# Performance work log

Measured on AMD Instinct MI355X. Metric: run time of the kernel, lower is better.

The kernel has to match this reference:

```python
import jax, jax.numpy as jnp
import numpy as np

B, S, NN = 16, 512, 8          # batch, spatial nodes, neighbors per node
IN, H, NHEAD = 128, 512, 4     # input_size, hidden_size, n_head


def _forward(inputs, h, c, h_spatial, a_src, w_fg, b_fg, w_ig, b_ig,
             w_ih, w_hh, b_ih, b_hh):
    N = B * S
    x = inputs.reshape(N, IN)
    h = h.reshape(N, H)
    c = c.reshape(N, H)
    hs = h_spatial.reshape(N, NN, H)

    # attention logits: concat(h, neighbor) @ a_src, split to avoid materializing concat
    a_self, a_nb = a_src[:H], a_src[H:]              # [H, NHEAD] each
    attn = h @ a_self                                  # [N, NHEAD]
    attn = attn[:, None, :] + jnp.einsum('nkh,hm->nkm', hs, a_nb)  # [N, NN, NHEAD]
    attn = jnp.where(attn >= 0, attn, 0.2 * attn)      # leaky_relu(0.2)
    attn = jax.nn.softmax(attn, axis=1)                # softmax over neighbors

    # aggregate neighbors per head -> [N, NHEAD*H]
    agg = jnp.einsum('nkm,nkh->nmh', attn, hs).reshape(N, NHEAD * H)

    spatial_f = jax.nn.sigmoid(agg @ w_fg.T + b_fg)    # [N, H]
    spatial_i = jax.nn.sigmoid(agg @ w_ig.T + b_ig)
    h = h * spatial_i
    c = c * spatial_f

    # torch LSTMCell: gate order i, f, g, o
    gates = x @ w_ih.T + b_ih + h @ w_hh.T + b_hh      # [N, 4H]
    i_g, f_g, g_g, o_g = jnp.split(gates, 4, axis=1)
    i_g = jax.nn.sigmoid(i_g)
    f_g = jax.nn.sigmoid(f_g)
    g_g = jnp.tanh(g_g)
    o_g = jax.nn.sigmoid(o_g)
    c_new = f_g * c + i_g * g_g
    h_new = o_g * jnp.tanh(c_new)
    return h_new.reshape(B, S, H), c_new.reshape(B, S, H)


def setup_inputs() -> dict:
    key = jax.random.key(0)
    ks = jax.random.split(key, 16)
    xav = lambda k, shp: jax.random.uniform(
        k, shp, jnp.float32, -1.0, 1.0) * np.sqrt(6.0 / (shp[0] + shp[1]))
    return {
        'inputs': jax.random.normal(ks[0], (B, S, IN), jnp.float32),
        'h': jax.random.normal(ks[1], (B, S, H), jnp.float32),
        'c': jax.random.normal(ks[2], (B, S, H), jnp.float32),
        'h_spatial': jax.random.normal(ks[3], (B, S, NN, H), jnp.float32),
        'a_src': xav(ks[4], (2 * H, NHEAD)),
        'w_fg': jax.random.normal(ks[5], (H, NHEAD * H), jnp.float32) * 0.02,
        'b_fg': jnp.zeros((H,), jnp.float32),
        'w_ig': jax.random.normal(ks[6], (H, NHEAD * H), jnp.float32) * 0.02,
        'b_ig': jnp.zeros((H,), jnp.float32),
        'w_ih': jax.random.normal(ks[7], (4 * H, IN), jnp.float32) * 0.02,
        'w_hh': jax.random.normal(ks[8], (4 * H, H), jnp.float32) * 0.02,
        'b_ih': jnp.zeros((4 * H,), jnp.float32),
        'b_hh': jnp.zeros((4 * H,), jnp.float32),
    }


def reference(inputs, h, c, h_spatial, a_src, w_fg, b_fg, w_ig, b_ig,
              w_ih, w_hh, b_ih, b_hh):
    return _forward(inputs, h, c, h_spatial, a_src, w_fg, b_fg, w_ig, b_ig,
                    w_ih, w_hh, b_ih, b_hh)
```

## Files before the change

### kernel.cpp

```cpp
#include <hip/hip_runtime.h>
#include <hip/hip_bf16.h>
#include <cstdint>
#include <cstddef>

#define N_ROWS 8192
#define HDIM 512
#define INDIM 128
#define NHEADS 4
#define NNB 8

typedef __bf16 bf16_t;
typedef __bf16 bf16x8 __attribute__((ext_vector_type(8)));
typedef __bf16 bf16x4 __attribute__((ext_vector_type(4)));
typedef __bf16 bf16x2 __attribute__((ext_vector_type(2)));
typedef float f32x4 __attribute__((ext_vector_type(4)));

__device__ __forceinline__ float sigmoidf_(float x) { return 1.0f / (1.0f + expf(-x)); }

__device__ __forceinline__ void load_lds16(const void* g, void* l) {
  __builtin_amdgcn_global_load_lds(
      (const __attribute__((address_space(1))) void*)g,
      (__attribute__((address_space(3))) void*)l, 16, 0, 0);
}

__global__ __launch_bounds__(256) void pack_kernel(
    const float* __restrict__ w_fg, const float* __restrict__ w_ig,
    const float* __restrict__ w_ih, const float* __restrict__ w_hh,
    const float* __restrict__ b_ih, const float* __restrict__ b_hh,
    const float* __restrict__ x,
    bf16_t* __restrict__ W1, bf16_t* __restrict__ W2i,
    float* __restrict__ b2, bf16_t* __restrict__ A2)
{
  int idx = blockIdx.x * 256 + threadIdx.x;
  if (idx < 524288) {
    const int e = idx * 4, r = e >> 11, k = e & 2047;
    const float* src = (r < 512) ? &w_fg[(size_t)r * 2048 + k]
                                 : &w_ig[(size_t)(r - 512) * 2048 + k];
    const float4 v = *(const float4*)src;
    bf16x4 o; o[0] = (bf16_t)v.x; o[1] = (bf16_t)v.y; o[2] = (bf16_t)v.z; o[3] = (bf16_t)v.w;
    *(bf16x4*)&W1[e] = o;
    return;
  }
  idx -= 524288;
  if (idx < 327680) {
    const int e = idx * 4, r = e / 640, k = e - r * 640;
    const int rp = (r & 511) * 4 + (r >> 9);
    const float* src = (k < 128) ? &w_ih[(size_t)r * 128 + k]
                                 : &w_hh[(size_t)r * 512 + (k - 128)];
    const float4 v = *(const float4*)src;
    bf16x4 o; o[0] = (bf16_t)v.x; o[1] = (bf16_t)v.y; o[2] = (bf16_t)v.z; o[3] = (bf16_t)v.w;
    *(bf16x4*)&W2i[(size_t)rp * 640 + k] = o;
    return;
  }
  idx -= 327680;
  if (idx < 2048) {
    const int q = idx >> 2, g = idx & 3;
    b2[idx] = b_ih[g * 512 + q] + b_hh[g * 512 + q];
    return;
  }
  idx -= 2048;
  if (idx < 262144) {
    const int e = idx * 4, n = e >> 7, cc = e & 127;
    const float4 v = *(const float4*)&x[e];
    bf16x4 o; o[0] = (bf16_t)v.x; o[1] = (bf16_t)v.y; o[2] = (bf16_t)v.z; o[3] = (bf16_t)v.w;
    *(bf16x4*)&A2[(size_t)n * 640 + cc] = o;
  }
}

__global__ __launch_bounds__(256) void attn_agg_kernel(
    const float* __restrict__ h, const float* __restrict__ hs,
    const float* __restrict__ a_src, bf16_t* __restrict__ agg)
{
  __shared__ float s_hs[NNB][HDIM];
  __shared__ float s_h[HDIM];
  __shared__ float s_logit[NNB][NHEADS];
  __shared__ float s_self[NHEADS];

  const int n = blockIdx.x;
  const int t = threadIdx.x;
  const float* hs_n = hs + (size_t)n * (NNB * HDIM);
  const float* h_n  = h  + (size_t)n * HDIM;

  {
    const float4* s4 = (const float4*)hs_n;
    float4* d4 = (float4*)&s_hs[0][0];
#pragma unroll
    for (int i = 0; i < 4; ++i) d4[t + i * 256] = s4[t + i * 256];
    if (t < HDIM / 4) ((float4*)s_h)[t] = ((const float4*)h_n)[t];
  }
  __syncthreads();

  const int wave = t >> 6, lane = t & 63;
#pragma unroll
  for (int kk = 0; kk < 2; ++kk) {
    const int k = wave * 2 + kk;
    float acc0 = 0.f, acc1 = 0.f, acc2 = 0.f, acc3 = 0.f;
#pragma unroll
    for (int i = 0; i < HDIM / 64; ++i) {
      const int hh = i * 64 + lane;
      const float v = s_hs[k][hh];
      const float4 av = *(const float4*)(a_src + (size_t)(HDIM + hh) * NHEADS);
      acc0 += v * av.x; acc1 += v * av.y; acc2 += v * av.z; acc3 += v * av.w;
    }
    float accs[NHEADS] = {acc0, acc1, acc2, acc3};
#pragma unroll
    for (int m = 0; m < NHEADS; ++m) {
      float a = accs[m];
#pragma unroll
      for (int off = 32; off > 0; off >>= 1) a += __shfl_xor(a, off);
      if (lane == 0) s_logit[k][m] = a;
    }
  }
  if (wave == 0) {
    float acc0 = 0.f, acc1 = 0.f, acc2 = 0.f, acc3 = 0.f;
#pragma unroll
    for (int i = 0; i < HDIM / 64; ++i) {
      const int hh = i * 64 + lane;
      const float v = s_h[hh];
      const float4 av = *(const float4*)(a_src + (size_t)hh * NHEADS);
      acc0 += v * av.x; acc1 += v * av.y; acc2 += v * av.z; acc3 += v * av.w;
    }
    float accs[NHEADS] = {acc0, acc1, acc2, acc3};
#pragma unroll
    for (int m = 0; m < NHEADS; ++m) {
      float a = accs[m];
#pragma unroll
      for (int off = 32; off > 0; off >>= 1) a += __shfl_xor(a, off);
      if (lane == 0) s_self[m] = a;
    }
  }
  __syncthreads();

  float w[NNB][NHEADS];
#pragma unroll
  for (int m = 0; m < NHEADS; ++m) {
    const float sm = s_self[m];
    float mx = -1e30f;
#pragma unroll
    for (int k = 0; k < NNB; ++k) {
      float l = sm + s_logit[k][m];
      l = (l >= 0.f) ? l : 0.2f * l;
      w[k][m] = l;
      mx = fmaxf(mx, l);
    }
    float sum = 0.f;
#pragma unroll
    for (int k = 0; k < NNB; ++k) { const float e = expf(w[k][m] - mx); w[k][m] = e; sum += e; }
    const float inv = 1.f / sum;
#pragma unroll
    for (int k = 0; k < NNB; ++k) w[k][m] *= inv;
  }

  bf16_t* agg_n = agg + (size_t)n * (NHEADS * HDIM);
  const int hh = t * 2;
  float e0[NNB], e1[NNB];
#pragma unroll
  for (int k = 0; k < NNB; ++k) { e0[k] = s_hs[k][hh]; e1[k] = s_hs[k][hh + 1]; }
#pragma unroll
  for (int m = 0; m < NHEADS; ++m) {
    float a0 = 0.f, a1 = 0.f;
#pragma unroll
    for (int k = 0; k < NNB; ++k) { a0 += w[k][m] * e0[k]; a1 += w[k][m] * e1[k]; }
    bf16x2 pk; pk[0] = (bf16_t)a0; pk[1] = (bf16_t)a1;
    *(bf16x2*)(agg_n + m * HDIM + hh) = pk;
  }
}

__global__ __launch_bounds__(256) void gemm1_kernel(
    const bf16_t* __restrict__ A, const bf16_t* __restrict__ Bt,
    const float* __restrict__ b_fg, const float* __restrict__ b_ig,
    const float* __restrict__ c_in, const float* __restrict__ h_in,
    float* __restrict__ cprime, bf16_t* __restrict__ A2)
{
  __shared__ bf16_t At[2][128][32];
  __shared__ bf16_t Bs[2][64][32];

  const int tid  = threadIdx.x;
  const int wave = tid >> 6, lane = tid & 63;
  const int wr = wave >> 1, wc = wave & 1;
  const int bm0 = blockIdx.x * 128;
  const int bn0 = blockIdx.y * 64;
  const int K = 2048;

  f32x4 acc[4][2] = {};

  const int srow = tid >> 2;
  const int sch  = tid & 3;
  const int gsw8 = (sch ^ ((srow >> 1) & 3)) * 8;
  const int sch8 = sch * 8;
  const int frow = lane & 15;
  const int fro8 = ((lane >> 4) ^ ((frow >> 1) & 3)) * 8;

  auto STAGE = [&](int buf, int k0) {
    load_lds16(A  + (size_t)(bm0 + srow)      * K + k0 + gsw8, &At[buf][srow][sch8]);
    load_lds16(A  + (size_t)(bm0 + 64 + srow) * K + k0 + gsw8, &At[buf][64 + srow][sch8]);
    load_lds16(Bt + (size_t)(bn0 + srow)      * K + k0 + gsw8, &Bs[buf][srow][sch8]);
  };
  auto COMPUTE = [&](int buf) {
    bf16x8 af[4], bv[2];
#pragma unroll
    for (int i = 0; i < 4; ++i) af[i] = *(const bf16x8*)&At[buf][wr * 64 + i * 16 + frow][fro8];
#pragma unroll
    for (int j = 0; j < 2; ++j) bv[j] = *(const bf16x8*)&Bs[buf][wc * 32 + j * 16 + frow][fro8];
#pragma unroll
    for (int i = 0; i < 4; ++i)
#pragma unroll
      for (int j = 0; j < 2; ++j)
        acc[i][j] = __builtin_amdgcn_mfma_f32_16x16x32_bf16(af[i], bv[j], acc[i][j], 0, 0, 0);
  };

  const int nt = K >> 5;
  STAGE(0, 0);
  __syncthreads();
  for (int t = 0; t < nt; ++t) {
    if (t + 1 < nt) STAGE((t + 1) & 1, (t + 1) * 32);
    COMPUTE(t & 1);
    __syncthreads();
  }

  const int col_in = lane & 15;
  const int row_in = (lane >> 4) * 4;
#pragma unroll
  for (int i = 0; i < 4; ++i) {
#pragma unroll
    for (int j = 0; j < 2; ++j) {
      const int col = bn0 + wc * 32 + j * 16 + col_in;
#pragma unroll
      for (int r = 0; r < 4; ++r) {
        const int row = bm0 + wr * 64 + i * 16 + row_in + r;
        const float v = acc[i][j][r];
        if (col < 512) {
          const float s = sigmoidf_(v + b_fg[col]);
          cprime[(size_t)row * 512 + col] = c_in[(size_t)row * 512 + col] * s;
        } else {
          const int jj = col - 512;
          const float s = sigmoidf_(v + b_ig[jj]);
          A2[(size_t)row * 640 + 128 + jj] = (bf16_t)(h_in[(size_t)row * 512 + jj] * s);
        }
      }
    }
  }
}

__global__ __launch_bounds__(256) void gemm2_kernel(
    const bf16_t* __restrict__ A, const bf16_t* __restrict__ Bt,
    const float* __restrict__ b2, const float* __restrict__ cprime,
    float* __restrict__ out)
{
  __shared__ union {
    struct { bf16_t A[2][128][32]; bf16_t B[2][128][32]; } st;
    float epi[64][128];
  } sm;

  const int tid  = threadIdx.x;
  const int wave = tid >> 6, lane = tid & 63;
  const int wr = wave >> 1, wc = wave & 1;
  const int bm0 = blockIdx.x * 128;
  const int bn0 = blockIdx.y * 128;
  const int K = 640;

  f32x4 acc[4][4] = {};

  const int srow = tid >> 2;
  const int sch  = tid & 3;
  const int gsw8 = (sch ^ ((srow >> 1) & 3)) * 8;
  const int sch8 = sch * 8;
  const int frow = lane & 15;
  const int fro8 = ((lane >> 4) ^ ((frow >> 1) & 3)) * 8;

  auto STAGE = [&](int buf, int k0) {
    load_lds16(A  + (size_t)(bm0 + srow)      * K + k0 + gsw8, &sm.st.A[buf][srow][sch8]);
    load_lds16(A  + (size_t)(bm0 + 64 + srow) * K + k0 + gsw8, &sm.st.A[buf][64 + srow][sch8]);
    load_lds16(Bt + (size_t)(bn0 + srow)      * K + k0 + gsw8, &sm.st.B[buf][srow][sch8]);
    load_lds16(Bt + (size_t)(bn0 + 64 + srow) * K + k0 + gsw8, &sm.st.B[buf][64 + srow][sch8]);
  };
  auto COMPUTE = [&](int buf) {
    bf16x8 af[4], bv[4];
#pragma unroll
    for (int i = 0; i < 4; ++i) af[i] = *(const bf16x8*)&sm.st.A[buf][wr * 64 + i * 16 + frow][fro8];
#pragma unroll
    for (int j = 0; j < 4; ++j) bv[j] = *(const bf16x8*)&sm.st.B[buf][wc * 64 + j * 16 + frow][fro8];
#pragma unroll
    for (int i = 0; i < 4; ++i)
#pragma unroll
      for (int j = 0; j < 4; ++j)
        acc[i][j] = __builtin_amdgcn_mfma_f32_16x16x32_bf16(af[i], bv[j], acc[i][j], 0, 0, 0);
  };

  const int nt = K >> 5;
  STAGE(0, 0);
  __syncthreads();
  for (int t = 0; t < nt; ++t) {
    if (t + 1 < nt) STAGE((t + 1) & 1, (t + 1) * 32);
    COMPUTE(t & 1);
    __syncthreads();
  }

  const int col_in = lane & 15;
  const int row_in = (lane >> 4) * 4;
  const int q0i = bn0 >> 2;
  const int qi  = tid & 31;
  const int r0  = tid >> 5;

#pragma unroll
  for (int p = 0; p < 2; ++p) {
    if (wr == p) {
#pragma unroll
      for (int i = 0; i < 4; ++i)
#pragma unroll
        for (int j = 0; j < 4; ++j)
#pragma unroll
          for (int r = 0; r < 4; ++r)
            sm.epi[i * 16 + row_in + r][wc * 64 + j * 16 + col_in] = acc[i][j][r];
    }
    __syncthreads();
    const float4 bb = *(const float4*)&b2[(size_t)(q0i + qi) * 4];
#pragma unroll
    for (int rr = 0; rr < 8; ++rr) {
      const int lr = r0 + rr * 8;
      const float4 g4 = *(const float4*)&sm.epi[lr][qi * 4];
      const int grow = bm0 + p * 64 + lr;
      const int q    = q0i + qi;
      const float cp = cprime[(size_t)grow * 512 + q];
      const float ig = sigmoidf_(g4.x + bb.x);
      const float fg = sigmoidf_(g4.y + bb.y);
      const float gg = tanhf(g4.z + bb.z);
      const float og = sigmoidf_(g4.w + bb.w);
      const float cn = fg * cp + ig * gg;
      const float hn = og * tanhf(cn);
      out[(size_t)grow * 512 + q] = hn;
      out[(size_t)N_ROWS * 512 + (size_t)grow * 512 + q] = cn;
    }
    __syncthreads();
  }
}

extern "C" void kernel_launch(void* const* d_in, const int* in_sizes, int n_in,
                              void* d_out, int out_size, void* d_ws, size_t ws_size,
                              hipStream_t stream) {
  const float* x     = (const float*)d_in[0];
  const float* h     = (const float*)d_in[1];
  const float* c     = (const float*)d_in[2];
  const float* hsp   = (const float*)d_in[3];
  const float* a_src = (const float*)d_in[4];
  const float* w_fg  = (const float*)d_in[5];
  const float* b_fg  = (const float*)d_in[6];
  const float* w_ig  = (const float*)d_in[7];
  const float* b_ig  = (const float*)d_in[8];
  const float* w_ih  = (const float*)d_in[9];
  const float* w_hh  = (const float*)d_in[10];
  const float* b_ih  = (const float*)d_in[11];
  const float* b_hh  = (const float*)d_in[12];
  float* out = (float*)d_out;

  uint8_t* ws = (uint8_t*)d_ws;
  bf16_t* agg    = (bf16_t*)(ws);
  bf16_t* W1     = (bf16_t*)(ws + 33554432);
  bf16_t* W2i    = (bf16_t*)(ws + 37748736);
  float*  b2     = (float*) (ws + 40370176);
  bf16_t* A2     = (bf16_t*)(ws + 40378368);
  float*  cprime = (float*) (ws + 50864128);

  pack_kernel<<<4360, 256, 0, stream>>>(w_fg, w_ig, w_ih, w_hh, b_ih, b_hh, x,
                                        W1, W2i, b2, A2);
  attn_agg_kernel<<<N_ROWS, 256, 0, stream>>>(h, hsp, a_src, agg);
  gemm1_kernel<<<dim3(64, 16), 256, 0, stream>>>(
      agg, W1, b_fg, b_ig, c, h, cprime, A2);
  gemm2_kernel<<<dim3(64, 16), 256, 0, stream>>>(
      A2, W2i, b2, cprime, out);
}
```

Baseline: 188.8 us.

## Use triple-buffered LDS staging with partial vmcnt waits in both GEMMs

Both GEMM kernels move from a double-buffered global-to-LDS pipeline with a full __syncthreads each step to a three-stage ring buffer. Explicit s_waitcnt vmcnt(N) waits only for the oldest stage, so two stages of loads stay in flight while the MFMAs run. This is meant to hide global load latency better in the K loops. In exchange the kernels use more LDS, which may reduce occupancy, and correctness now depends on the hand-counted outstanding-load numbers.

```diff
diff --git a/kernel.cpp b/kernel.cpp
--- a/kernel.cpp
+++ b/kernel.cpp
@@ -172,8 +172,8 @@
     const float* __restrict__ c_in, const float* __restrict__ h_in,
     float* __restrict__ cprime, bf16_t* __restrict__ A2)
 {
-  __shared__ bf16_t At[2][128][32];
-  __shared__ bf16_t Bs[2][64][32];
+  __shared__ bf16_t At[3][128][32];
+  __shared__ bf16_t Bs[3][64][32];
 
   const int tid  = threadIdx.x;
   const int wave = tid >> 6, lane = tid & 63;
@@ -208,15 +208,35 @@
       for (int j = 0; j < 2; ++j)
         acc[i][j] = __builtin_amdgcn_mfma_f32_16x16x32_bf16(af[i], bv[j], acc[i][j], 0, 0, 0);
   };
+  auto WAIT_BAR = [&](int n_outstanding) {
+    if (n_outstanding == 6) asm volatile("s_waitcnt vmcnt(6)" ::: "memory");
+    else if (n_outstanding == 3) asm volatile("s_waitcnt vmcnt(3)" ::: "memory");
+    else asm volatile("s_waitcnt vmcnt(0)" ::: "memory");
+    __builtin_amdgcn_s_barrier();
+    __builtin_amdgcn_sched_barrier(0);
+  };
+  auto END_BAR = [&]() {
+    __builtin_amdgcn_sched_barrier(0);
+    __builtin_amdgcn_s_barrier();
+    __builtin_amdgcn_sched_barrier(0);
+  };
 
   const int nt = K >> 5;
-  STAGE(0, 0);
-  __syncthreads();
-  for (int t = 0; t < nt; ++t) {
-    if (t + 1 < nt) STAGE((t + 1) & 1, (t + 1) * 32);
-    COMPUTE(t & 1);
-    __syncthreads();
-  }
+  STAGE(0, 0); STAGE(1, 32); STAGE(2, 64);
+  for (int t = 0; t < nt - 3; ++t) {
+    WAIT_BAR(6);
+    COMPUTE(t % 3);
+    END_BAR();
+    STAGE(t % 3, (t + 3) * 32);
+  }
+  WAIT_BAR(6);
+  COMPUTE((nt - 3) % 3);
+  END_BAR();
+  WAIT_BAR(3);
+  COMPUTE((nt - 2) % 3);
+  END_BAR();
+  WAIT_BAR(0);
+  COMPUTE((nt - 1) % 3);
 
   const int col_in = lane & 15;
   const int row_in = (lane >> 4) * 4;
@@ -248,7 +268,7 @@
     float* __restrict__ out)
 {
   __shared__ union {
-    struct { bf16_t A[2][128][32]; bf16_t B[2][128][32]; } st;
+    struct { bf16_t A[3][128][32]; bf16_t B[3][128][32]; } st;
     float epi[64][128];
   } sm;
 
@@ -286,15 +306,37 @@
       for (int j = 0; j < 4; ++j)
         acc[i][j] = __builtin_amdgcn_mfma_f32_16x16x32_bf16(af[i], bv[j], acc[i][j], 0, 0, 0);
   };
+  auto WAIT_BAR = [&](int n_outstanding) {
+    if (n_outstanding == 8) asm volatile("s_waitcnt vmcnt(8)" ::: "memory");
+    else if (n_outstanding == 4) asm volatile("s_waitcnt vmcnt(4)" ::: "memory");
+    else asm volatile("s_waitcnt vmcnt(0)" ::: "memory");
+    __builtin_amdgcn_s_barrier();
+    __builtin_amdgcn_sched_barrier(0);
+  };
+  auto END_BAR = [&]() {
+    __builtin_amdgcn_sched_barrier(0);
+    __builtin_amdgcn_s_barrier();
+    __builtin_amdgcn_sched_barrier(0);
+  };
 
   const int nt = K >> 5;
-  STAGE(0, 0);
+  STAGE(0, 0); STAGE(1, 32); STAGE(2, 64);
+  for (int t = 0; t < nt - 3; ++t) {
+    WAIT_BAR(8);
+    COMPUTE(t % 3);
+    END_BAR();
+    STAGE(t % 3, (t + 3) * 32);
+  }
+  WAIT_BAR(8);
+  COMPUTE((nt - 3) % 3);
+  END_BAR();
+  WAIT_BAR(4);
+  COMPUTE((nt - 2) % 3);
+  END_BAR();
+  WAIT_BAR(0);
+  COMPUTE((nt - 1) % 3);
+
   __syncthreads();
-  for (int t = 0; t < nt; ++t) {
-    if (t + 1 < nt) STAGE((t + 1) & 1, (t + 1) * 32);
-    COMPUTE(t & 1);
-    __syncthreads();
-  }
 
   const int col_in = lane & 15;
   const int row_in = (lane >> 4) * 4;
```

After: 186.6 us. About the same (-1.2%).
